# Kernel tuning notes

Hardware: AMD Instinct MI355X
Metric: run time of the kernel (lower is better)

## Reference

```python
import jax, jax.numpy as jnp
import numpy as np

H = 32        # num attention heads
KVH = 8       # num key/value heads
HD = 64       # head dim
D = H * HD    # hidden size 2048
EPS = 1e-6
ROPE_THETA = 10000.0
MAX_POS = 2048


def rotate_half(x):
    x1, x2 = jnp.split(x, 2, axis=-1)
    return jnp.concatenate((-x2, x1), axis=-1)


def rms_norm(x, w):
    # per-head RMSNorm over last dim, computed in fp32 like the torch module
    x32 = x.astype(jnp.float32)
    inv = jax.lax.rsqrt(jnp.mean(x32 * x32, axis=-1, keepdims=True) + EPS)
    return w * (x32 * inv).astype(x.dtype)


def setup_inputs() -> dict:
    key = jax.random.key(0)
    ks = jax.random.split(key, 6)
    B, S = 2, 2048
    hidden_states = jax.random.normal(ks[0], (B, S, D), dtype=jnp.float32)
    # rotary tables [MAX_POS, HD]
    inv_freq = 1.0 / (ROPE_THETA ** (np.arange(0, HD, 2, dtype=np.float32) / HD))
    t = np.arange(MAX_POS, dtype=np.float32)
    freqs = np.outer(t, inv_freq)                      # [MAX_POS, HD/2]
    emb = np.concatenate([freqs, freqs], axis=-1)      # [MAX_POS, HD]
    cos = jnp.asarray(np.cos(emb))
    sin = jnp.asarray(np.sin(emb))
    scale = 1.0 / np.sqrt(D)
    wq = jax.random.normal(ks[1], (D, D), dtype=jnp.float32) * scale
    wk = jax.random.normal(ks[2], (D, KVH * HD), dtype=jnp.float32) * scale
    wv = jax.random.normal(ks[3], (D, KVH * HD), dtype=jnp.float32) * scale
    wo = jax.random.normal(ks[4], (D, D), dtype=jnp.float32) * scale
    q_ln_w = jnp.ones((HD,), dtype=jnp.float32)
    k_ln_w = jnp.ones((HD,), dtype=jnp.float32)
    return {"hidden_states": hidden_states, "cos": cos, "sin": sin,
            "wq": wq, "wk": wk, "wv": wv, "wo": wo,
            "q_ln_w": q_ln_w, "k_ln_w": k_ln_w}


def reference(hidden_states, cos, sin, wq, wk, wv, wo, q_ln_w, k_ln_w):
    B, S, _ = hidden_states.shape
    n_rep = H // KVH
    q = (hidden_states @ wq).reshape(B, S, H, HD)
    k = (hidden_states @ wk).reshape(B, S, KVH, HD)
    v = (hidden_states @ wv).reshape(B, S, KVH, HD)
    # per-head RMSNorm on q/k, then to (B, heads, S, HD)
    q = rms_norm(q, q_ln_w).transpose(0, 2, 1, 3)
    k = rms_norm(k, k_ln_w).transpose(0, 2, 1, 3)
    v = v.transpose(0, 2, 1, 3)
    # RoPE
    c = cos[:S][None, None]  # [1,1,S,HD]
    s = sin[:S][None, None]
    q = q * c + rotate_half(q) * s
    k = k * c + rotate_half(k) * s
    # GQA: repeat kv heads
    k = jnp.repeat(k, n_rep, axis=1)
    v = jnp.repeat(v, n_rep, axis=1)
    scores = jnp.einsum('bhqd,bhkd->bhqk', q, k) / np.sqrt(HD)
    causal = jnp.tril(jnp.ones((S, S), dtype=bool))
    scores = jnp.where(causal, scores, -jnp.inf)
    p = jax.nn.softmax(scores.astype(jnp.float32), axis=-1).astype(q.dtype)
    out = jnp.einsum('bhqk,bhkd->bhqd', p, v)
    out = out.transpose(0, 2, 1, 3).reshape(B, S, D)
    return out @ wo
```

## Files before the change

kernel.cpp:

```cpp
#include <hip/hip_runtime.h>
#include <hip/hip_bf16.h>

#define HH 32
#define KVHN 8
#define HD 64
#define DMODEL 2048
#define SEQ 2048
#define BB 2
#define NTOK 4096
#define DKV 512
#define NQKV 3072

typedef __bf16 bf16x8 __attribute__((ext_vector_type(8)));
typedef __bf16 bf16x4 __attribute__((ext_vector_type(4)));
typedef float  f32x4  __attribute__((ext_vector_type(4)));

typedef const __attribute__((address_space(1))) void gvoid_t;
typedef __attribute__((address_space(3))) void lvoid_t;

__device__ inline void glds16(const void* g, void* l) {
  __builtin_amdgcn_global_load_lds((gvoid_t*)g, (lvoid_t*)l, 16, 0, 0);
}

__device__ inline f32x4 mfma16(bf16x8 a, bf16x8 b, f32x4 c) {
  return __builtin_amdgcn_mfma_f32_16x16x32_bf16(a, b, c, 0, 0, 0);
}

__device__ inline float fast_exp2(float x) {
  float r;
  asm("v_exp_f32 %0, %1" : "=v"(r) : "v"(x));
  return r;
}


__global__ __launch_bounds__(256)
void k_prep(const float* __restrict__ hidden, __bf16* __restrict__ Abf,
            const float* __restrict__ wq, const float* __restrict__ wk,
            const float* __restrict__ wv, const float* __restrict__ wo,
            __bf16* __restrict__ WT, __bf16* __restrict__ WoT) {
  __shared__ float tile[32][33];
  const int id = blockIdx.x, tid = threadIdx.x;
  if (id < 8192) {
    int i = (id * 256 + tid) * 4;
    f32x4 v = *(const f32x4*)(hidden + i);
    bf16x4 o;
    o[0] = (__bf16)v[0]; o[1] = (__bf16)v[1];
    o[2] = (__bf16)v[2]; o[3] = (__bf16)v[3];
    *(bf16x4*)(Abf + i) = o;
    return;
  }
  const float* W; __bf16* T; int K, N, n0, k0;
  if (id < 12288) {
    int t = id - 8192; W = wq; T = WT; K = 2048; N = 2048;
    n0 = (t & 63) * 32; k0 = (t >> 6) * 32;
  } else if (id < 14336) {
    int t = id - 12288; int z = t >> 10;
    W = z ? wv : wk; T = WT + (size_t)(2048 + z * 512) * 2048;
    K = 2048; N = 512;
    n0 = (t & 15) * 32; k0 = ((t >> 4) & 63) * 32;
  } else {
    int t = id - 14336; W = wo; T = WoT; K = 2048; N = 2048;
    n0 = (t & 63) * 32; k0 = (t >> 6) * 32;
  }
  int tx = tid & 31, ty = tid >> 5;
#pragma unroll
  for (int i = 0; i < 32; i += 8)
    tile[ty + i][tx] = W[(size_t)(k0 + ty + i) * N + n0 + tx];
  __syncthreads();
#pragma unroll
  for (int i = 0; i < 32; i += 8)
    T[(size_t)(n0 + ty + i) * K + k0 + tx] = (__bf16)tile[tx][ty + i];
}


__device__ inline void stc(float* p, float v)  { *p = v; }
__device__ inline void stc(__bf16* p, float v) { *p = (__bf16)v; }

template <int EPI, typename CT>
__global__ __launch_bounds__(256, 4)
void k_gemm3(const __bf16* __restrict__ A, const __bf16* __restrict__ BT,
             CT* __restrict__ C, int M, int N, int K,
             const float* __restrict__ cosT, const float* __restrict__ sinT,
             const float* __restrict__ qw, const float* __restrict__ kw,
             __bf16* __restrict__ Qr, __bf16* __restrict__ Kr,
             __bf16* __restrict__ Vt) {
  __shared__ alignas(16) __bf16 Al[2][128 * 32];
  __shared__ alignas(16) __bf16 Bl[2][128 * 32];
  const int tid = threadIdx.x;
  const int wid = tid >> 6, lane = tid & 63, g = lane >> 4, r16 = lane & 15;
  const int wm = wid >> 1, wn = wid & 1;
  const int nbm = M >> 7, nbn = N >> 7;
  const int nwg = nbm * nbn;
  int id = blockIdx.x;
  id = (id & 7) * (nwg >> 3) + (id >> 3);
  const int bm = id % nbm, bn = id / nbm;

  const int pp = tid >> 3;
  const int c8 = (tid & 7) ^ (pp & 7);
  const int sr1 = 2 * pp + (c8 >> 2);
  const int sr2 = 64 + sr1;
  const int c1 = (c8 & 3) * 8;
  const __bf16* gA1 = A + (size_t)(bm * 128 + sr1) * K + c1;
  const __bf16* gA2 = A + (size_t)(bm * 128 + sr2) * K + c1;
  const __bf16* gB1 = BT + (size_t)(bn * 128 + sr1) * K + c1;
  const __bf16* gB2 = BT + (size_t)(bn * 128 + sr2) * K + c1;

  int aoff[4], boff[4];
#pragma unroll
  for (int m = 0; m < 4; ++m) {
    int row = wm * 64 + m * 16 + r16;
    aoff[m] = (row >> 1) * 64 + (((((row & 1) << 2) | g) ^ ((row >> 1) & 7)) * 8);
  }
#pragma unroll
  for (int n = 0; n < 4; ++n) {
    int row = wn * 64 + n * 16 + r16;
    boff[n] = (row >> 1) * 64 + (((((row & 1) << 2) | g) ^ ((row >> 1) & 7)) * 8);
  }

  auto STAGE = [&](int sl, int kt) {
    const int ko = kt * 32;
    glds16(gA1 + ko, &Al[sl][tid * 8]);
    glds16(gA2 + ko, &Al[sl][2048 + tid * 8]);
    glds16(gB1 + ko, &Bl[sl][tid * 8]);
    glds16(gB2 + ko, &Bl[sl][2048 + tid * 8]);
  };

  f32x4 acc[4][4] = {};
  const int nk = K >> 5;

  STAGE(0, 0);
  for (int kt = 0; kt < nk; ++kt) {
    const int s = kt & 1;
    if (kt + 1 < nk) {
      STAGE(s ^ 1, kt + 1);
      asm volatile("s_waitcnt vmcnt(4)" ::: "memory");
    } else {
      asm volatile("s_waitcnt vmcnt(0)" ::: "memory");
    }
    __builtin_amdgcn_s_barrier();
    bf16x8 af[4], bfr[4];
#pragma unroll
    for (int m = 0; m < 4; ++m) af[m] = *(const bf16x8*)&Al[s][aoff[m]];
#pragma unroll
    for (int n = 0; n < 4; ++n) bfr[n] = *(const bf16x8*)&Bl[s][boff[n]];
    __builtin_amdgcn_s_setprio(1);
#pragma unroll
    for (int m = 0; m < 4; ++m)
#pragma unroll
      for (int n = 0; n < 4; ++n)
        acc[m][n] = mfma16(af[m], bfr[n], acc[m][n]);
    __builtin_amdgcn_s_setprio(0);
    __builtin_amdgcn_s_barrier();
  }

  if (EPI == 0) {
#pragma unroll
    for (int m = 0; m < 4; ++m) {
      int row = bm * 128 + wm * 64 + m * 16 + g * 4;
#pragma unroll
      for (int n = 0; n < 4; ++n) {
        int col = bn * 128 + wn * 64 + n * 16 + r16;
#pragma unroll
        for (int r = 0; r < 4; ++r)
          stc(&C[(size_t)(row + r) * N + col], acc[m][n][r]);
      }
    }
  } else {
    const int colbase = bn * 128 + wn * 64;
    const float QSCALE = 0.18033688011112042f;
    if (colbase < DMODEL + DKV) {
      const bool isq = colbase < DMODEL;
      const float* wp = isq ? qw : kw;
      const float qs = isq ? QSCALE : 1.0f;
      float w4[4];
#pragma unroll
      for (int n = 0; n < 4; ++n) w4[n] = wp[n * 16 + r16];
#pragma unroll
      for (int m = 0; m < 4; ++m) {
        const int rowm = bm * 128 + wm * 64 + m * 16 + g * 4;
        float ss[4];
#pragma unroll
        for (int r = 0; r < 4; ++r) {
          ss[r] = acc[m][0][r] * acc[m][0][r] + acc[m][1][r] * acc[m][1][r] +
                  acc[m][2][r] * acc[m][2][r] + acc[m][3][r] * acc[m][3][r];
#pragma unroll
          for (int mk = 1; mk < 16; mk <<= 1) ss[r] += __shfl_xor(ss[r], mk);
          ss[r] = rsqrtf(ss[r] * (1.0f / HD) + 1e-6f);
        }
#pragma unroll
        for (int r = 0; r < 4; ++r) {
          const int t = rowm + r;
          const int sidx = t & (SEQ - 1);
          const float inv_ = ss[r];
#pragma unroll
          for (int n = 0; n < 4; ++n) {
            const int d = n * 16 + r16;
            const float xn = acc[m][n][r] * inv_ * w4[n];
            const float xp = acc[m][n ^ 2][r] * inv_ * w4[n ^ 2];
            const float rot = (n < 2) ? -xp : xp;
            const float cv = cosT[sidx * HD + d], sv = sinT[sidx * HD + d];
            const float o = (xn * cv + rot * sv) * qs;
            if (isq) {
              const int hq = colbase >> 6;
              Qr[((size_t)t * HH + hq) * HD + d] = (__bf16)o;
            } else {
              const int kvh = (colbase - DMODEL) >> 6;
              Kr[((size_t)t * KVHN + kvh) * HD + d] = (__bf16)o;
            }
          }
        }
      }
    } else {
      const int vc0 = colbase - (DMODEL + DKV);
#pragma unroll
      for (int m = 0; m < 4; ++m) {
        const int rowm = bm * 128 + wm * 64 + m * 16 + g * 4;
        const int bb2 = rowm >> 11;
        const int s0 = rowm & (SEQ - 1);
#pragma unroll
        for (int n = 0; n < 4; ++n) {
          const int c = vc0 + n * 16 + r16;
          bf16x4 pk;
#pragma unroll
          for (int r = 0; r < 4; ++r) pk[r] = (__bf16)acc[m][n][r];
          *(bf16x4*)&Vt[((size_t)bb2 * DKV + c) * SEQ + s0] = pk;
        }
      }
    }
  }
}


__global__ __launch_bounds__(512)
void k_attn(const __bf16* __restrict__ Q, const __bf16* __restrict__ Kg,
            const __bf16* __restrict__ VT, __bf16* __restrict__ O) {
  __shared__ alignas(16) __bf16 Kl[2][64 * 64];
  __shared__ alignas(16) __bf16 Vl[2][64 * 64];
  __shared__ alignas(16) __bf16 Pl[8][16 * 72];
  const int f = blockIdx.x;
  const int b = f >> 8;
  const int h = (f & 255) >> 3;
  const int j = f & 7;
  const int kvh = h >> 2;
  const int tid = threadIdx.x, wid = tid >> 6, lane = tid & 63;
  const int g = lane >> 4, r16 = lane & 15;
  __bf16* Pw = Pl[wid];

  const int rr = lane >> 3;
  const int cc = (lane & 7) ^ rr;

  auto STAGE = [&](int buf, int kb) {
    const int krow = kb * 64 + wid * 8 + rr;
    glds16(&Kg[((size_t)(b * SEQ + krow) * KVHN + kvh) * HD + cc * 8],
           &Kl[buf][wid * 512]);
    const int d = wid * 8 + rr;
    glds16(&VT[(size_t)(b * DKV + kvh * HD + d) * SEQ + (size_t)kb * 64 + cc * 8],
           &Vl[buf][wid * 512]);
  };

#pragma unroll 1
  for (int phase = 0; phase < 2; ++phase) {
    const int qt = phase ? j : 15 - j;
    const int q0 = qt * 128 + wid * 16;
    const int ntile = 2 * qt + 2;

    bf16x8 qf[2];
#pragma unroll
    for (int h2 = 0; h2 < 2; ++h2)
      qf[h2] = *(const bf16x8*)&Q[(((size_t)b * SEQ + q0 + r16) * HH + h) * HD + h2 * 32 + g * 8];

    f32x4 acc[4] = {};
    float l_q = 0.0f;

    STAGE(0, 0);
    asm volatile("s_waitcnt vmcnt(0)" ::: "memory");
    __syncthreads();

    for (int kb = 0; kb < ntile; ++kb) {
      const int cur = kb & 1;
      if (kb + 1 < ntile) STAGE(cur ^ 1, kb + 1);
      const __bf16* Kb = Kl[cur];
      const __bf16* Vb = Vl[cur];
      if (kb * 64 <= q0 + 15) {
        bf16x8 kf[4][2];
#pragma unroll
        for (int ks = 0; ks < 4; ++ks)
#pragma unroll
          for (int h2 = 0; h2 < 2; ++h2) {
            const int p = r16 + ks * 16;
            const int ch = (g + 4 * h2) ^ (p & 7);
            kf[ks][h2] = *(const bf16x8*)&Kb[p * 64 + ch * 8];
          }
        const bool needmask = (kb * 64 + 63 > q0);
        float svv[4][4];
        __builtin_amdgcn_s_setprio(1);
#pragma unroll
        for (int ks = 0; ks < 4; ++ks) {
          f32x4 sacc = {-12.f, -12.f, -12.f, -12.f};
          sacc = mfma16(kf[ks][0], qf[0], sacc);
          sacc = mfma16(kf[ks][1], qf[1], sacc);
#pragma unroll
          for (int r = 0; r < 4; ++r) svv[ks][r] = sacc[r];
        }
        __builtin_amdgcn_s_setprio(0);
        if (needmask) {
#pragma unroll
          for (int ks = 0; ks < 4; ++ks)
#pragma unroll
            for (int r = 0; r < 4; ++r) {
              int pg = kb * 64 + ks * 16 + g * 4 + r;
              int qg = q0 + r16;
              if (pg > qg) svv[ks][r] = -1e30f;
            }
        }
#pragma unroll
        for (int ks = 0; ks < 4; ++ks) {
          bf16x4 pk;
#pragma unroll
          for (int r = 0; r < 4; ++r) {
            float p = fast_exp2(svv[ks][r]);
            l_q += p;
            pk[r] = (__bf16)p;
          }
          *(bf16x4*)&Pw[r16 * 72 + ks * 16 + g * 4] = pk;
        }
        bf16x8 pf0 = *(const bf16x8*)&Pw[r16 * 72 + g * 8];
        bf16x8 pf1 = *(const bf16x8*)&Pw[r16 * 72 + 32 + g * 8];
        __builtin_amdgcn_s_setprio(1);
#pragma unroll
        for (int nb = 0; nb < 4; ++nb) {
          const int d = r16 + nb * 16;
          const int ch0 = g ^ (d & 7), ch1 = (4 + g) ^ (d & 7);
          bf16x8 vf0 = *(const bf16x8*)&Vb[d * 64 + ch0 * 8];
          bf16x8 vf1 = *(const bf16x8*)&Vb[d * 64 + ch1 * 8];
          acc[nb] = mfma16(pf0, vf0, acc[nb]);
          acc[nb] = mfma16(pf1, vf1, acc[nb]);
        }
        __builtin_amdgcn_s_setprio(0);
      }
      asm volatile("s_waitcnt vmcnt(0)" ::: "memory");
      __syncthreads();
    }
    l_q += __shfl_xor(l_q, 16);
    l_q += __shfl_xor(l_q, 32);
    const float invq = 1.0f / l_q;
    float inv[4];
#pragma unroll
    for (int r = 0; r < 4; ++r) inv[r] = __shfl(invq, g * 4 + r);
#pragma unroll
    for (int nb = 0; nb < 4; ++nb)
#pragma unroll
      for (int r = 0; r < 4; ++r)
        O[(((size_t)b * SEQ + q0 + g * 4 + r) * HH + h) * HD + nb * 16 + r16] =
            (__bf16)(acc[nb][r] * inv[r]);
  }
}


extern "C" void kernel_launch(void* const* d_in, const int* in_sizes, int n_in,
                              void* d_out, int out_size, void* d_ws, size_t ws_size,
                              hipStream_t stream) {
  const float* hidden = (const float*)d_in[0];
  const float* cosT   = (const float*)d_in[1];
  const float* sinT   = (const float*)d_in[2];
  const float* wq     = (const float*)d_in[3];
  const float* wk     = (const float*)d_in[4];
  const float* wv     = (const float*)d_in[5];
  const float* wo     = (const float*)d_in[6];
  const float* qw     = (const float*)d_in[7];
  const float* kw     = (const float*)d_in[8];
  float* out = (float*)d_out;
  char* ws = (char*)d_ws;

  __bf16* Abf  = (__bf16*)(ws);
  __bf16* Ob   = Abf;
  __bf16* WT   = (__bf16*)(ws + (16u << 20));
  __bf16* Qr   = (__bf16*)(ws + (28u << 20));
  __bf16* Kr   = (__bf16*)(ws + (44u << 20));
  __bf16* VT   = (__bf16*)(ws + (52u << 20));
  __bf16* WoT  = (__bf16*)(ws + (56u << 20));

  k_prep<<<18432, 256, 0, stream>>>(hidden, Abf, wq, wk, wv, wo, WT, WoT);

  k_gemm3<1, __bf16><<<768, 256, 0, stream>>>(Abf, WT, (__bf16*)nullptr,
      NTOK, NQKV, DMODEL, cosT, sinT, qw, kw, Qr, Kr, VT);

  k_attn<<<dim3(512), 512, 0, stream>>>(Qr, Kr, VT, Ob);

  k_gemm3<0, float><<<512, 256, 0, stream>>>(Ob, WoT, out,
      NTOK, DMODEL, DMODEL, nullptr, nullptr, nullptr, nullptr,
      nullptr, nullptr, nullptr);
}
```

Baseline: 186.2 us.

## Add 256x256-tile 8-wave QKV GEMM with interleaved ping-pong LDS prefetch

Adds a new k_gemm8 kernel that has 512 threads compute a 256x256 output tile with K-steps of 64. It keeps even and odd LDS buffers for A and B, and issues the global-to-LDS loads for the next K-steps in pieces between the MFMA phases. The fused RMSNorm/RoPE/V-transpose epilogue moves to this kernel and is used for the QKV projection, while k_gemm3 is reduced to a plain store epilogue for the output projection. The bigger tile raises data reuse per load, but the grid shrinks to 192 workgroups, which may not fill all CUs. LDS use is large at 128KB per block, and register pressure rises.

```diff
diff --git a/kernel.cpp b/kernel.cpp
--- a/kernel.cpp
+++ b/kernel.cpp
@@ -79,11 +79,7 @@
 template <int EPI, typename CT>
 __global__ __launch_bounds__(256, 4)
 void k_gemm3(const __bf16* __restrict__ A, const __bf16* __restrict__ BT,
-             CT* __restrict__ C, int M, int N, int K,
-             const float* __restrict__ cosT, const float* __restrict__ sinT,
-             const float* __restrict__ qw, const float* __restrict__ kw,
-             __bf16* __restrict__ Qr, __bf16* __restrict__ Kr,
-             __bf16* __restrict__ Vt) {
+             CT* __restrict__ C, int M, int N, int K) {
   __shared__ alignas(16) __bf16 Al[2][128 * 32];
   __shared__ alignas(16) __bf16 Bl[2][128 * 32];
   const int tid = threadIdx.x;
@@ -153,20 +149,141 @@
     __builtin_amdgcn_s_barrier();
   }
 
+#pragma unroll
+  for (int m = 0; m < 4; ++m) {
+    int row = bm * 128 + wm * 64 + m * 16 + g * 4;
+#pragma unroll
+    for (int n = 0; n < 4; ++n) {
+      int col = bn * 128 + wn * 64 + n * 16 + r16;
+#pragma unroll
+      for (int r = 0; r < 4; ++r)
+        stc(&C[(size_t)(row + r) * N + col], acc[m][n][r]);
+    }
+  }
+}
+
+
+template <int EPI, typename CT>
+__global__ __launch_bounds__(512, 2)
+void k_gemm8(const __bf16* __restrict__ A, const __bf16* __restrict__ BT,
+             CT* __restrict__ C, int M, int N, int K,
+             const float* __restrict__ cosT, const float* __restrict__ sinT,
+             const float* __restrict__ qw, const float* __restrict__ kw,
+             __bf16* __restrict__ Qr, __bf16* __restrict__ Kr,
+             __bf16* __restrict__ Vt) {
+  __shared__ alignas(16) __bf16 AlE[256 * 64];
+  __shared__ alignas(16) __bf16 AlO[256 * 64];
+  __shared__ alignas(16) __bf16 BlE[256 * 64];
+  __shared__ alignas(16) __bf16 BlO[256 * 64];
+  const int tid = threadIdx.x;
+  const int wid = tid >> 6, lane = tid & 63, g = lane >> 4, r16 = lane & 15;
+  const int wm = wid >> 2, wn = wid & 3;
+  const int nbm = M >> 8, nbn = N >> 8;
+  const int nwg = nbm * nbn;
+  int id = blockIdx.x;
+  id = (id & 7) * (nwg >> 3) + (id >> 3);
+  const int bm = id % nbm, bn = id / nbm;
+
+  const int srow = tid >> 3;
+  const int schunk = tid & 7;
+  const int sc = (schunk ^ (srow & 7)) * 8;
+  const __bf16* gA = A + (size_t)(bm * 256 + srow) * K + sc;
+  const __bf16* gB = BT + (size_t)(bn * 256 + srow) * K + sc;
+
+  auto SA = [&](__bf16* buf, int kt, int q) {
+    glds16(gA + (size_t)q * 64 * K + kt * 64,
+           &buf[(q * 64 + srow) * 64 + schunk * 8]);
+  };
+  auto SB = [&](__bf16* buf, int kt, int q) {
+    glds16(gB + (size_t)q * 64 * K + kt * 64,
+           &buf[(q * 64 + srow) * 64 + schunk * 8]);
+  };
+
+  const int cs0 = (g ^ (r16 & 7)) * 8;
+  const int cs1 = ((4 + g) ^ (r16 & 7)) * 8;
+
+  f32x4 acc[8][4] = {};
+  const int nk = K >> 6;
+
+  SA(AlE, 0, 0); SA(AlE, 0, 1); SA(AlE, 0, 2); SA(AlE, 0, 3);
+  SB(BlE, 0, 0); SB(BlE, 0, 1); SB(BlE, 0, 2); SB(BlE, 0, 3);
+  SB(BlO, 1, 0); SB(BlO, 1, 1); SB(BlO, 1, 2); SB(BlO, 1, 3);
+  asm volatile("s_waitcnt vmcnt(4)" ::: "memory");
+  __builtin_amdgcn_s_barrier();
+
+#pragma unroll 1
+  for (int i = 0; i < (nk >> 1); ++i) {
+    const int t = 2 * i;
+    const bool s2 = (t + 2 < nk), s3 = (t + 3 < nk);
+    bf16x8 bfr[4][2];
+#pragma unroll
+    for (int p = 0; p < 8; ++p) {
+      const __bf16* Ab = (p < 4) ? AlE : AlO;
+      const __bf16* Bb = (p < 4) ? BlE : BlO;
+      const int mp = p & 3;
+      bf16x8 af[2][2];
+#pragma unroll
+      for (int j = 0; j < 2; ++j) {
+        const int row = wm * 128 + (2 * mp + j) * 16 + r16;
+        af[j][0] = *(const bf16x8*)&Ab[row * 64 + cs0];
+        af[j][1] = *(const bf16x8*)&Ab[row * 64 + cs1];
+      }
+      if (mp == 0) {
+#pragma unroll
+        for (int n = 0; n < 4; ++n) {
+          const int row = wn * 64 + n * 16 + r16;
+          bfr[n][0] = *(const bf16x8*)&Bb[row * 64 + cs0];
+          bfr[n][1] = *(const bf16x8*)&Bb[row * 64 + cs1];
+        }
+      }
+      asm volatile("" ::: "memory");
+      switch (p) {
+        case 0: SA(AlO, t + 1, 0); SA(AlO, t + 1, 1); break;
+        case 1: SA(AlO, t + 1, 2); SA(AlO, t + 1, 3); break;
+        case 2: if (s2) { SB(BlE, t + 2, 0); SB(BlE, t + 2, 1); } break;
+        case 3: if (s2) { SB(BlE, t + 2, 2); SB(BlE, t + 2, 3); } break;
+        case 4: if (s2) { SA(AlE, t + 2, 0); SA(AlE, t + 2, 1); } break;
+        case 5: if (s2) { SA(AlE, t + 2, 2); SA(AlE, t + 2, 3); } break;
+        case 6: if (s3) { SB(BlO, t + 3, 0); SB(BlO, t + 3, 1); } break;
+        case 7: if (s3) { SB(BlO, t + 3, 2); SB(BlO, t + 3, 3); } break;
+      }
+      if (p == 3) {
+        if (s2) asm volatile("s_waitcnt vmcnt(4)" ::: "memory");
+        else    asm volatile("s_waitcnt vmcnt(0)" ::: "memory");
+      }
+      if (p == 7) {
+        if (s3) asm volatile("s_waitcnt vmcnt(4)" ::: "memory");
+        else    asm volatile("s_waitcnt vmcnt(0)" ::: "memory");
+      }
+      __builtin_amdgcn_s_barrier();
+      asm volatile("s_waitcnt lgkmcnt(0)" ::: "memory");
+      __builtin_amdgcn_s_setprio(1);
+#pragma unroll
+      for (int j = 0; j < 2; ++j)
+#pragma unroll
+        for (int n = 0; n < 4; ++n) {
+          acc[2 * mp + j][n] = mfma16(af[j][0], bfr[n][0], acc[2 * mp + j][n]);
+          acc[2 * mp + j][n] = mfma16(af[j][1], bfr[n][1], acc[2 * mp + j][n]);
+        }
+      __builtin_amdgcn_s_setprio(0);
+      __builtin_amdgcn_s_barrier();
+    }
+  }
+
   if (EPI == 0) {
 #pragma unroll
-    for (int m = 0; m < 4; ++m) {
-      int row = bm * 128 + wm * 64 + m * 16 + g * 4;
+    for (int m = 0; m < 8; ++m) {
+      int row = bm * 256 + wm * 128 + m * 16 + g * 4;
 #pragma unroll
       for (int n = 0; n < 4; ++n) {
-        int col = bn * 128 + wn * 64 + n * 16 + r16;
+        int col = bn * 256 + wn * 64 + n * 16 + r16;
 #pragma unroll
         for (int r = 0; r < 4; ++r)
           stc(&C[(size_t)(row + r) * N + col], acc[m][n][r]);
       }
     }
   } else {
-    const int colbase = bn * 128 + wn * 64;
+    const int colbase = bn * 256 + wn * 64;
     const float QSCALE = 0.18033688011112042f;
     if (colbase < DMODEL + DKV) {
       const bool isq = colbase < DMODEL;
@@ -176,8 +293,8 @@
 #pragma unroll
       for (int n = 0; n < 4; ++n) w4[n] = wp[n * 16 + r16];
 #pragma unroll
-      for (int m = 0; m < 4; ++m) {
-        const int rowm = bm * 128 + wm * 64 + m * 16 + g * 4;
+      for (int m = 0; m < 8; ++m) {
+        const int rowm = bm * 256 + wm * 128 + m * 16 + g * 4;
         float ss[4];
 #pragma unroll
         for (int r = 0; r < 4; ++r) {
@@ -213,8 +330,8 @@
     } else {
       const int vc0 = colbase - (DMODEL + DKV);
 #pragma unroll
-      for (int m = 0; m < 4; ++m) {
-        const int rowm = bm * 128 + wm * 64 + m * 16 + g * 4;
+      for (int m = 0; m < 8; ++m) {
+        const int rowm = bm * 256 + wm * 128 + m * 16 + g * 4;
         const int bb2 = rowm >> 11;
         const int s0 = rowm & (SEQ - 1);
 #pragma unroll
@@ -382,12 +499,11 @@
 
   k_prep<<<18432, 256, 0, stream>>>(hidden, Abf, wq, wk, wv, wo, WT, WoT);
 
-  k_gemm3<1, __bf16><<<768, 256, 0, stream>>>(Abf, WT, (__bf16*)nullptr,
+  k_gemm8<1, __bf16><<<192, 512, 0, stream>>>(Abf, WT, (__bf16*)nullptr,
       NTOK, NQKV, DMODEL, cosT, sinT, qw, kw, Qr, Kr, VT);
 
   k_attn<<<dim3(512), 512, 0, stream>>>(Qr, Kr, VT, Ob);
 
   k_gemm3<0, float><<<512, 256, 0, stream>>>(Ob, WoT, out,
-      NTOK, DMODEL, DMODEL, nullptr, nullptr, nullptr, nullptr,
-      nullptr, nullptr, nullptr);
-}
+      NTOK, DMODEL, DMODEL);
+}
```

After: 185.1 us. Within noise of the previous version (-0.6%).
